# Performance work log

Measured on AMD Instinct MI355X. Metric: run time of the kernel, lower is better.

The kernel has to match this reference:

```python
import jax, jax.numpy as jnp
import numpy as np

D_MODEL = 512
H = 8
DH = D_MODEL // H
P = H * (H - 1) // 2  # 28 head pairs
THRESH = 0.1
B, N = 2, 2048

# pair indices (i<j) in the same row-major order as the nested torch loop
_I_IDX, _J_IDX = np.triu_indices(H, k=1)
I_IDX = jnp.asarray(_I_IDX)
J_IDX = jnp.asarray(_J_IDX)


def setup_inputs() -> dict:
    key = jax.random.key(0)
    ks = jax.random.split(key, 10)
    s = 1.0 / np.sqrt(D_MODEL)
    return {
        "x": jax.random.normal(ks[0], (B, N, D_MODEL), dtype=jnp.float32),
        "Wq": jax.random.normal(ks[1], (D_MODEL, D_MODEL), dtype=jnp.float32) * s,
        "bq": jnp.zeros((D_MODEL,), dtype=jnp.float32),
        "Wk": jax.random.normal(ks[2], (D_MODEL, D_MODEL), dtype=jnp.float32) * s,
        "bk": jnp.zeros((D_MODEL,), dtype=jnp.float32),
        "Wv": jax.random.normal(ks[3], (D_MODEL, D_MODEL), dtype=jnp.float32) * s,
        "bv": jnp.zeros((D_MODEL,), dtype=jnp.float32),
        "Wo": jax.random.normal(ks[4], (D_MODEL, D_MODEL), dtype=jnp.float32) * s,
        "bo": jnp.zeros((D_MODEL,), dtype=jnp.float32),
        # stacked restriction maps: (P, DH_out, DH_in), Linear(bias=False)
        "Wr": jax.random.normal(ks[5], (P, DH, DH), dtype=jnp.float32) / np.sqrt(DH),
        "agreement_scale": jnp.asarray(1.0, dtype=jnp.float32),
    }


def reference(x, Wq, bq, Wk, bk, Wv, bv, Wo, bo, Wr, agreement_scale):
    b, n, d = x.shape
    # projections (torch Linear: y = x @ W.T + b), split into heads -> (B,H,N,DH)
    q = (x @ Wq.T + bq).reshape(b, n, H, DH).transpose(0, 2, 1, 3)
    k = (x @ Wk.T + bk).reshape(b, n, H, DH).transpose(0, 2, 1, 3)
    v = (x @ Wv.T + bv).reshape(b, n, H, DH).transpose(0, 2, 1, 3)

    scores = jnp.einsum("bhnd,bhmd->bhnm", q, k) / jnp.sqrt(jnp.asarray(DH, x.dtype))
    attn = jax.nn.softmax(scores, axis=-1)
    head_out = jnp.einsum("bhnm,bhmd->bhnd", attn, v)  # (B,H,N,DH)

    # --- pairwise restriction-map agreement, fully batched over the P pairs ---
    hi = head_out[:, I_IDX]  # (B,P,N,DH)
    hj = head_out[:, J_IDX]  # (B,P,N,DH)
    ri = jnp.einsum("bpnd,ped->bpne", hi, Wr)  # per-pair Linear(bias=False)
    diff = jnp.linalg.norm(ri - hj, axis=-1).mean(axis=-1)  # (B,P)
    score = jnp.exp(-diff * agreement_scale / THRESH)  # (B,P)

    agreement = jnp.zeros((b, H, H), dtype=x.dtype)
    agreement = agreement.at[:, I_IDX, J_IDX].set(score)
    agreement = agreement.at[:, J_IDX, I_IDX].set(score)
    diag = jnp.arange(H)
    agreement = agreement.at[:, diag, diag].set(1.0)

    # --- consensus aggregation ---
    offdiag = 1.0 - jnp.eye(H, dtype=x.dtype)
    consensus = (agreement * offdiag).sum(axis=-1) / (H - 1)  # (B,H)
    filtered = consensus * (consensus > THRESH).astype(x.dtype)
    weights = jax.nn.softmax(filtered + 1e-10, axis=-1)  # (B,H)

    agg = (head_out * weights[:, :, None, None]).sum(axis=1)  # (B,N,DH)
    agg = jnp.tile(agg, (1, 1, H))  # torch .repeat(1,1,H) -> (B,N,D)
    return agg @ Wo.T + bo
```

## Files before the change

### kernel.cpp

```cpp
#include <hip/hip_runtime.h>
#include <hip/hip_bf16.h>
#include <stdint.h>

typedef __attribute__((ext_vector_type(8))) short bf16x8;
typedef __attribute__((ext_vector_type(4))) float f32x4;
typedef __attribute__((ext_vector_type(4))) unsigned short u16x4;

#define LDS_SWZ(row, col) (((((col) >> 3) ^ ((row) & 7)) << 4))

__device__ __forceinline__ unsigned short f2bf(float f) {
  union { float f; unsigned u; } v; v.f = f;
  unsigned r = v.u + 0x7FFFu + ((v.u >> 16) & 1u);
  return (unsigned short)(r >> 16);
}
__device__ __forceinline__ float bf2f(unsigned short h) {
  union { unsigned u; float f; } v; v.u = ((unsigned)h) << 16;
  return v.f;
}
__device__ __forceinline__ unsigned pk2bf(float a, float b) {
  __hip_bfloat162 h2 = __float22bfloat162_rn(float2{a, b});
  unsigned u; __builtin_memcpy(&u, &h2, 4); return u;
}
__device__ __forceinline__ void gld_lds16(const void* g, void* l) {
  __builtin_amdgcn_global_load_lds((const __attribute__((address_space(1))) void*)g,
                                   (__attribute__((address_space(3))) void*)l, 16, 0, 0);
}

__global__ void k_prep(const float* __restrict__ x, const float* __restrict__ wq,
                       const float* __restrict__ wk, const float* __restrict__ wv,
                       const float* __restrict__ wr, const float* __restrict__ wo,
                       unsigned short* __restrict__ xb, unsigned short* __restrict__ wb,
                       unsigned short* __restrict__ wrb, unsigned short* __restrict__ wsb) {
  int q = blockIdx.x * blockDim.x + threadIdx.x;
  if (q >= 749568) {
    int t = q - 749568;
    if (t >= 512 * 64) return;
    int e = t >> 6, d = t & 63;
    float s = 0.f;
#pragma unroll
    for (int qq = 0; qq < 8; ++qq) s += wo[e * 512 + qq * 64 + d];
    wsb[t] = f2bf(s);
    return;
  }
  const float* src; unsigned short* dst; int off;
  if (q < 524288)      { src = x;  dst = xb;          off = q; }
  else if (q < 589824) { src = wq; dst = wb;          off = q - 524288; }
  else if (q < 655360) { src = wk; dst = wb + 262144; off = q - 589824; }
  else if (q < 720896) { src = wv; dst = wb + 524288; off = q - 655360; }
  else                 { src = wr; dst = wrb;         off = q - 720896; }
  float4 v = ((const float4*)src)[off];
  u16x4 o; o.x = f2bf(v.x); o.y = f2bf(v.y); o.z = f2bf(v.z); o.w = f2bf(v.w);
  ((u16x4*)dst)[off] = o;
}

__global__ __launch_bounds__(256) void k_qkv(
    const unsigned short* __restrict__ xb, const unsigned short* __restrict__ wb,
    const float* __restrict__ bq, const float* __restrict__ bk, const float* __restrict__ bv,
    unsigned short* __restrict__ qb, unsigned short* __restrict__ kb,
    unsigned short* __restrict__ vtb) {
  __shared__ alignas(16) unsigned char As[2][128 * 128];
  __shared__ alignas(16) unsigned char Bs[2][64 * 128];
  const int tid = threadIdx.x;
  const int wave = tid >> 6, lane = tid & 63;
  const int rowbase = blockIdx.x * 128;
  const int colbase = blockIdx.y * 64;
  const int z = blockIdx.z;
  const unsigned short* W = wb + z * 512 * 512;
  const float* bias = (z == 0) ? bq : ((z == 1) ? bk : bv);
  f32x4 acc[2][4] = {};

#define QKV_STAGE(buf, kt_)                                                            \
  do {                                                                                 \
    _Pragma("unroll") for (int i_ = 0; i_ < 4; ++i_) {                                 \
      const int L_ = i_ * 256 + tid;                                                   \
      const int row_ = L_ >> 3, pos_ = L_ & 7;                                         \
      gld_lds16(xb + (rowbase + row_) * 512 + (kt_) * 64 + ((pos_ ^ (row_ & 7)) << 3), \
                As[buf] + (i_ * 256 + wave * 64) * 16);                                \
    }                                                                                  \
    _Pragma("unroll") for (int i_ = 0; i_ < 2; ++i_) {                                 \
      const int L_ = i_ * 256 + tid;                                                   \
      const int row_ = L_ >> 3, pos_ = L_ & 7;                                         \
      gld_lds16(W + (colbase + row_) * 512 + (kt_) * 64 + ((pos_ ^ (row_ & 7)) << 3),  \
                Bs[buf] + (i_ * 256 + wave * 64) * 16);                                \
    }                                                                                  \
  } while (0)

  QKV_STAGE(0, 0);
  __syncthreads();
  for (int kt = 0; kt < 8; ++kt) {
    const int cur = kt & 1;
    if (kt < 7) QKV_STAGE(cur ^ 1, kt + 1);
#pragma unroll
    for (int kc = 0; kc < 2; ++kc) {
      bf16x8 af[2], bfr[4];
#pragma unroll
      for (int mq = 0; mq < 2; ++mq) {
        const int row = wave * 32 + mq * 16 + (lane & 15);
        const int col = kc * 32 + ((lane >> 4) << 3);
        af[mq] = *(const bf16x8*)(As[cur] + row * 128 + LDS_SWZ(row, col));
      }
#pragma unroll
      for (int nq = 0; nq < 4; ++nq) {
        const int row = nq * 16 + (lane & 15);
        const int col = kc * 32 + ((lane >> 4) << 3);
        bfr[nq] = *(const bf16x8*)(Bs[cur] + row * 128 + LDS_SWZ(row, col));
      }
#pragma unroll
      for (int mq = 0; mq < 2; ++mq)
#pragma unroll
        for (int nq = 0; nq < 4; ++nq)
          acc[mq][nq] = __builtin_amdgcn_mfma_f32_16x16x32_bf16(af[mq], bfr[nq], acc[mq][nq], 0, 0, 0);
    }
    __syncthreads();
  }
  const float qs = 0.18033688011112043f;
#pragma unroll
  for (int mq = 0; mq < 2; ++mq)
#pragma unroll
    for (int nq = 0; nq < 4; ++nq)
#pragma unroll
      for (int r = 0; r < 4; ++r) {
        const int grow = rowbase + wave * 32 + mq * 16 + ((lane >> 4) << 2) + r;
        const int col = colbase + nq * 16 + (lane & 15);
        float v = acc[mq][nq][r] + bias[col];
        const int b = grow >> 11, n = grow & 2047;
        const int h = col >> 6, dh = col & 63;
        if (z == 0)      qb[(((b << 3) + h) * 2048 + n) * 64 + dh] = f2bf(v * qs);
        else if (z == 1) kb[(((b << 3) + h) * 2048 + n) * 64 + dh] = f2bf(v);
        else             vtb[((((b << 3) + h) << 6) + dh) * 2048 + n] = f2bf(v);
      }
}

__global__ __launch_bounds__(512, 4) void k_attn(
    const unsigned short* __restrict__ qb, const unsigned short* __restrict__ kb,
    const unsigned short* __restrict__ vtb, unsigned short* __restrict__ hob) {
  __shared__ alignas(16) unsigned char smem[81920];
  const int tid = threadIdx.x, wave = tid >> 6, lane = tid & 63;
  const int team = wave >> 2, w4 = wave & 3;
  const int ttid = tid & 255;
  const int bh = blockIdx.x >> 5;
  const int qt = blockIdx.x & 31;
  const int n0 = qt * 64 + w4 * 16;
  const int lq = lane & 15, lg = lane >> 4;
  unsigned char* Kt = smem + team * 32768;
  unsigned char* Vt = Kt + 16384;
  unsigned char* pw = smem + 65536 + wave * 2048;
  const unsigned short* kbase = kb + bh * 2048 * 64;
  const unsigned short* vbase = vtb + bh * 64 * 2048;
  bf16x8 qf[2];
#pragma unroll
  for (int kc = 0; kc < 2; ++kc)
    qf[kc] = *(const bf16x8*)(qb + (bh * 2048 + n0 + lq) * 64 + kc * 32 + (lg << 3));
  f32x4 oacc[4] = {};
  float mrun = -1e30f, lpart = 0.f;

#define ATTN_STAGE(buf, T_)                                                        \
  do {                                                                             \
    _Pragma("unroll") for (int i_ = 0; i_ < 2; ++i_) {                             \
      const int L_ = i_ * 256 + ttid;                                              \
      const int row_ = L_ >> 3, pos_ = L_ & 7;                                     \
      gld_lds16(kbase + ((T_) * 64 + row_) * 64 + ((pos_ ^ (row_ & 7)) << 3),      \
                Kt + (buf) * 8192 + (i_ * 256 + w4 * 64) * 16);                    \
      gld_lds16(vbase + row_ * 2048 + (T_) * 64 + ((pos_ ^ (row_ & 7)) << 3),      \
                Vt + (buf) * 8192 + (i_ * 256 + w4 * 64) * 16);                    \
    }                                                                              \
  } while (0)

  ATTN_STAGE(0, team * 16);
  __syncthreads();
  for (int t = 0; t < 16; ++t) {
    const int cur = t & 1;
    if (t < 15) ATTN_STAGE(cur ^ 1, team * 16 + t + 1);
    f32x4 s[4];
#pragma unroll
    for (int mc = 0; mc < 4; ++mc) {
      f32x4 zz = {};
#pragma unroll
      for (int kc = 0; kc < 2; ++kc) {
        const int row = mc * 16 + lq;
        const int col = kc * 32 + (lg << 3);
        bf16x8 kf = *(const bf16x8*)(Kt + cur * 8192 + row * 128 + LDS_SWZ(row, col));
        zz = __builtin_amdgcn_mfma_f32_16x16x32_bf16(kf, qf[kc], zz, 0, 0, 0);
      }
      s[mc] = zz;
    }
    float lm = s[0][0];
#pragma unroll
    for (int mc = 0; mc < 4; ++mc)
#pragma unroll
      for (int r = 0; r < 4; ++r) lm = fmaxf(lm, s[mc][r]);
    if (__any(lm > mrun + 8.f)) {
      float v = fmaxf(lm, __shfl_xor(lm, 16));
      v = fmaxf(v, __shfl_xor(v, 32));
      float mnew = fmaxf(mrun, v);
      float sc = exp2f(mrun - mnew);
      mrun = mnew; lpart *= sc;
      float sco[4];
#pragma unroll
      for (int r = 0; r < 4; ++r) sco[r] = __shfl(sc, (lane & 48) | ((lg << 2) + r));
#pragma unroll
      for (int c2 = 0; c2 < 4; ++c2) {
        f32x4 o = oacc[c2];
#pragma unroll
        for (int r = 0; r < 4; ++r) o[r] *= sco[r];
        oacc[c2] = o;
      }
    }
    float pl[4][4];
#pragma unroll
    for (int mc = 0; mc < 4; ++mc) {
      float ps = 0.f;
#pragma unroll
      for (int r = 0; r < 4; ++r) { float p = exp2f(s[mc][r] - mrun); pl[mc][r] = p; ps += p; }
      lpart += ps;
      const int kk = mc * 16 + (lg << 2);
      uint2 pkd = { pk2bf(pl[mc][0], pl[mc][1]), pk2bf(pl[mc][2], pl[mc][3]) };
      *(uint2*)(pw + lq * 128 + LDS_SWZ(lq, kk) + ((kk & 7) << 1)) = pkd;
    }
    bf16x8 pa[2];
#pragma unroll
    for (int kc = 0; kc < 2; ++kc)
      pa[kc] = *(const bf16x8*)(pw + lq * 128 + LDS_SWZ(lq, kc * 32 + (lg << 3)));
#pragma unroll
    for (int c2 = 0; c2 < 4; ++c2) {
      f32x4 o = oacc[c2];
#pragma unroll
      for (int kc = 0; kc < 2; ++kc) {
        const int row = c2 * 16 + lq;
        const int col = kc * 32 + (lg << 3);
        bf16x8 vf = *(const bf16x8*)(Vt + cur * 8192 + row * 128 + LDS_SWZ(row, col));
        o = __builtin_amdgcn_mfma_f32_16x16x32_bf16(pa[kc], vf, o, 0, 0, 0);
      }
      oacc[c2] = o;
    }
    __syncthreads();
  }
  float ltot = lpart + __shfl_xor(lpart, 16);
  ltot += __shfl_xor(ltot, 32);
  float m_o[4], l_o[4];
#pragma unroll
  for (int r = 0; r < 4; ++r) {
    const int src = (lane & 48) | ((lg << 2) + r);
    m_o[r] = __shfl(mrun, src);
    l_o[r] = __shfl(ltot, src);
  }
  float* ex = (float*)smem;
  float* px = ex + (w4 * 64 + lane) * 25;
  if (team == 1) {
#pragma unroll
    for (int c2 = 0; c2 < 4; ++c2)
#pragma unroll
      for (int r = 0; r < 4; ++r) px[c2 * 4 + r] = oacc[c2][r];
#pragma unroll
    for (int r = 0; r < 4; ++r) { px[16 + r] = m_o[r]; px[20 + r] = l_o[r]; }
  }
  __syncthreads();
  if (team == 0) {
    float w0[4], w1[4];
#pragma unroll
    for (int r = 0; r < 4; ++r) {
      float m1 = px[16 + r], l1 = px[20 + r];
      float ms = fmaxf(m_o[r], m1);
      float a = exp2f(m_o[r] - ms), b = exp2f(m1 - ms);
      float li = 1.f / (a * l_o[r] + b * l1);
      w0[r] = a * li; w1[r] = b * li;
    }
#pragma unroll
    for (int c2 = 0; c2 < 4; ++c2)
#pragma unroll
      for (int r = 0; r < 4; ++r) {
        const int n = n0 + (lg << 2) + r;
        const int dh = c2 * 16 + lq;
        float o1 = px[c2 * 4 + r];
        hob[(bh * 2048 + n) * 64 + dh] = f2bf(w0[r] * oacc[c2][r] + w1[r] * o1);
      }
  }
}

__global__ __launch_bounds__(256) void k_pair(const unsigned short* __restrict__ hob,
                                              const unsigned short* __restrict__ wrb,
                                              float* __restrict__ dpart) {
  __shared__ alignas(16) unsigned char Ws[64 * 128];
  __shared__ alignas(16) unsigned char Hj[2][64 * 128];
  __shared__ float red[4];
  const int tid = threadIdx.x, wave = tid >> 6, lane = tid & 63;
  const int chunk = blockIdx.x & 7, bp = blockIdx.x >> 3;
  const int b = bp / 28, p = bp % 28;
  int pp = p, ii = 0;
  while (pp >= 7 - ii) { pp -= 7 - ii; ii++; }
  const int i = ii, j = ii + 1 + pp;
  const unsigned short* hib = hob + ((b * 8 + i) * 2048) * 64;
  const unsigned short* hjb = hob + ((b * 8 + j) * 2048) * 64;

#define PAIR_STAGE(buf, t_)                                                      \
  do {                                                                           \
    _Pragma("unroll") for (int is_ = 0; is_ < 2; ++is_) {                        \
      const int L_ = is_ * 256 + tid;                                            \
      const int row_ = L_ >> 3, pos_ = L_ & 7;                                   \
      gld_lds16(hjb + ((t_) * 64 + row_) * 64 + ((pos_ ^ (row_ & 7)) << 3),      \
                Hj[buf] + (is_ * 256 + wave * 64) * 16);                         \
    }                                                                            \
  } while (0)

#pragma unroll
  for (int is = 0; is < 2; ++is) {
    const int L = is * 256 + tid;
    const int row = L >> 3, pos = L & 7;
    gld_lds16(wrb + (p * 64 + row) * 64 + ((pos ^ (row & 7)) << 3), Ws + (is * 256 + wave * 64) * 16);
  }
  PAIR_STAGE(0, chunk * 4);
  __syncthreads();
  bf16x8 wf[4][2];
#pragma unroll
  for (int c = 0; c < 4; ++c)
#pragma unroll
    for (int kc = 0; kc < 2; ++kc) {
      const int row = c * 16 + (lane & 15);
      const int col = kc * 32 + ((lane >> 4) << 3);
      wf[c][kc] = *(const bf16x8*)(Ws + row * 128 + LDS_SWZ(row, col));
    }
  float wacc = 0.f;
  for (int t = 0; t < 4; ++t) {
    const int tt = chunk * 4 + t;
    const int cur = t & 1;
    if (t < 3) PAIR_STAGE(cur ^ 1, tt + 1);
    const int rbase = tt * 64 + wave * 16;
    f32x4 ri[4] = {};
#pragma unroll
    for (int kc = 0; kc < 2; ++kc) {
      bf16x8 hf = *(const bf16x8*)(hib + (rbase + (lane & 15)) * 64 + kc * 32 + ((lane >> 4) << 3));
#pragma unroll
      for (int c = 0; c < 4; ++c)
        ri[c] = __builtin_amdgcn_mfma_f32_16x16x32_bf16(hf, wf[c][kc], ri[c], 0, 0, 0);
    }
#pragma unroll
    for (int r = 0; r < 4; ++r) {
      const int row = wave * 16 + ((lane >> 4) << 2) + r;
      float ss = 0.f;
#pragma unroll
      for (int c = 0; c < 4; ++c) {
        const int col = c * 16 + (lane & 15);
        float hv = bf2f(*(const unsigned short*)(Hj[cur] + (row & 63) * 128 + LDS_SWZ(row & 63, col) + ((col & 7) << 1)));
        float d = ri[c][r] - hv;
        ss += d * d;
      }
#pragma unroll
      for (int off = 1; off < 16; off <<= 1) ss += __shfl_xor(ss, off);
      if ((lane & 15) == 0) wacc += sqrtf(ss);
    }
    __syncthreads();
  }
  float tot = __shfl(wacc, 0) + __shfl(wacc, 16) + __shfl(wacc, 32) + __shfl(wacc, 48);
  if (lane == 0) red[wave] = tot;
  __syncthreads();
  if (tid == 0) dpart[blockIdx.x] = red[0] + red[1] + red[2] + red[3];
}

__global__ __launch_bounds__(256) void k_agg(const unsigned short* __restrict__ hob,
                                             const float* __restrict__ dpart,
                                             const float* __restrict__ scal,
                                             unsigned short* __restrict__ aggb) {
  __shared__ float sc_s[2][28];
  __shared__ float filt[2][8];
  __shared__ float wts_s[16];
  const int tid = threadIdx.x;
  if (tid < 56) {
    int bb = tid / 28, pp = tid % 28;
    int base = (bb * 28 + pp) * 8;
    float diff = 0.f;
#pragma unroll
    for (int c = 0; c < 8; ++c) diff += dpart[base + c];
    diff /= 2048.f;
    sc_s[bb][pp] = expf(-diff * scal[0] / 0.1f);
  }
  __syncthreads();
  if (tid < 16) {
    int bb = tid / 8, h = tid % 8;
    float cons = 0.f;
    for (int h2 = 0; h2 < 8; ++h2)
      if (h2 != h) {
        int i_ = h < h2 ? h : h2, j_ = h < h2 ? h2 : h;
        int pp = i_ * (15 - i_) / 2 + (j_ - i_ - 1);
        cons += sc_s[bb][pp];
      }
    cons /= 7.f;
    filt[bb][h] = (cons > 0.1f) ? cons : 0.f;
  }
  __syncthreads();
  if (tid < 16) {
    int bb = tid / 8, h = tid % 8;
    float m = -1e30f;
    for (int h2 = 0; h2 < 8; ++h2) m = fmaxf(m, filt[bb][h2] + 1e-10f);
    float s = 0.f;
    for (int h2 = 0; h2 < 8; ++h2) s += expf(filt[bb][h2] + 1e-10f - m);
    wts_s[tid] = expf(filt[bb][h] + 1e-10f - m) / s;
  }
  __syncthreads();
  int t = blockIdx.x * blockDim.x + tid;
  if (t >= 4096 * 8) return;
  int r = t >> 3, dblk = t & 7;
  int b = r >> 11, n = r & 2047;
  float acc[8] = {};
#pragma unroll
  for (int h = 0; h < 8; ++h) {
    float w = wts_s[b * 8 + h];
    bf16x8 v = *(const bf16x8*)(hob + (((b * 8 + h) << 11) + n) * 64 + dblk * 8);
#pragma unroll
    for (int e = 0; e < 8; ++e) acc[e] += w * bf2f((unsigned short)v[e]);
  }
  bf16x8 o;
#pragma unroll
  for (int e = 0; e < 8; ++e) o[e] = (short)f2bf(acc[e]);
  *(bf16x8*)(aggb + r * 64 + dblk * 8) = o;
}

__global__ __launch_bounds__(256) void k_out(const unsigned short* __restrict__ aggb,
                                             const unsigned short* __restrict__ wsb,
                                             const float* __restrict__ bo,
                                             float* __restrict__ out) {
  __shared__ alignas(16) unsigned char Ws[64 * 128];
  const int tid = threadIdx.x, wave = tid >> 6, lane = tid & 63;
  const int rowb = blockIdx.x * 64, colb = blockIdx.y * 64;
#pragma unroll
  for (int is = 0; is < 2; ++is) {
    const int L = is * 256 + tid;
    const int row = L >> 3, pos = L & 7;
    gld_lds16(wsb + (colb + row) * 64 + ((pos ^ (row & 7)) << 3), Ws + (is * 256 + wave * 64) * 16);
  }
  __syncthreads();
  bf16x8 af[2];
#pragma unroll
  for (int kc = 0; kc < 2; ++kc)
    af[kc] = *(const bf16x8*)(aggb + (rowb + wave * 16 + (lane & 15)) * 64 + kc * 32 + ((lane >> 4) << 3));
  f32x4 acc[4] = {};
#pragma unroll
  for (int c = 0; c < 4; ++c)
#pragma unroll
    for (int kc = 0; kc < 2; ++kc) {
      const int row = c * 16 + (lane & 15);
      const int col = kc * 32 + ((lane >> 4) << 3);
      bf16x8 wfr = *(const bf16x8*)(Ws + row * 128 + LDS_SWZ(row, col));
      acc[c] = __builtin_amdgcn_mfma_f32_16x16x32_bf16(af[kc], wfr, acc[c], 0, 0, 0);
    }
#pragma unroll
  for (int c = 0; c < 4; ++c)
#pragma unroll
    for (int r = 0; r < 4; ++r) {
      const int grow = rowb + wave * 16 + ((lane >> 4) << 2) + r;
      const int col = colb + c * 16 + (lane & 15);
      out[grow * 512 + col] = acc[c][r] + bo[col];
    }
}

extern "C" void kernel_launch(void* const* d_in, const int* in_sizes, int n_in,
                              void* d_out, int out_size, void* d_ws, size_t ws_size,
                              hipStream_t stream) {
  const float* x  = (const float*)d_in[0];
  const float* Wq = (const float*)d_in[1];
  const float* bq = (const float*)d_in[2];
  const float* Wk = (const float*)d_in[3];
  const float* bk = (const float*)d_in[4];
  const float* Wv = (const float*)d_in[5];
  const float* bv = (const float*)d_in[6];
  const float* Wo = (const float*)d_in[7];
  const float* bo = (const float*)d_in[8];
  const float* Wr = (const float*)d_in[9];
  const float* ascale = (const float*)d_in[10];
  float* out = (float*)d_out;

  char* ws = (char*)d_ws;
  unsigned short* xb   = (unsigned short*)(ws);
  unsigned short* qb   = (unsigned short*)(ws + (4u << 20));
  unsigned short* kb   = (unsigned short*)(ws + (8u << 20));
  unsigned short* vtb  = (unsigned short*)(ws + (12u << 20));
  unsigned short* hob  = (unsigned short*)(ws + (16u << 20));
  unsigned short* wb   = (unsigned short*)(ws + (20u << 20));
  unsigned short* wrb  = (unsigned short*)(ws + (20u << 20) + 3u * 512 * 512 * 2);
  unsigned short* wsb  = (unsigned short*)(ws + (20u << 20) + 3u * 512 * 512 * 2 + 28u * 64 * 64 * 2);
  unsigned short* aggb = (unsigned short*)(ws + (22u << 20));
  float* dpart = (float*)(ws + (23u << 20));

  k_prep<<<3056, 256, 0, stream>>>(x, Wq, Wk, Wv, Wr, Wo, xb, wb, wrb, wsb);
  k_qkv<<<dim3(32, 8, 3), 256, 0, stream>>>(xb, wb, bq, bk, bv, qb, kb, vtb);
  k_attn<<<512, 512, 0, stream>>>(qb, kb, vtb, hob);
  k_pair<<<448, 256, 0, stream>>>(hob, wrb, dpart);
  k_agg<<<128, 256, 0, stream>>>(hob, dpart, ascale, aggb);
  k_out<<<dim3(64, 8), 256, 0, stream>>>(aggb, wsb, bo, out);
}
```

Measured before the change: 78.78 us.

## Process two query fragments per wave in attention to reuse K/V tiles

Each attention wave now handles 32 query rows (two 16-row fragments) instead of 16. Every K and V fragment read from LDS feeds two MFMAs, which halves the number of blocks and the K/V staging traffic per query. The change also adds s_setprio around the MFMA sections, uses a simpler unswizzled P layout in LDS, and interleaves blocks across heads. In exchange it needs more registers and 96KB of LDS per block, which lowers occupancy.

```diff
diff --git a/kernel.cpp b/kernel.cpp
--- a/kernel.cpp
+++ b/kernel.cpp
@@ -131,28 +131,30 @@
       }
 }
 
-__global__ __launch_bounds__(512, 4) void k_attn(
+__global__ __launch_bounds__(512, 2) void k_attn(
     const unsigned short* __restrict__ qb, const unsigned short* __restrict__ kb,
     const unsigned short* __restrict__ vtb, unsigned short* __restrict__ hob) {
-  __shared__ alignas(16) unsigned char smem[81920];
+  __shared__ alignas(16) unsigned char smem[98304];
   const int tid = threadIdx.x, wave = tid >> 6, lane = tid & 63;
-  const int team = wave >> 2, w4 = wave & 3;
+  const int team = wave >> 2, qsub = wave & 3;
   const int ttid = tid & 255;
-  const int bh = blockIdx.x >> 5;
-  const int qt = blockIdx.x & 31;
-  const int n0 = qt * 64 + w4 * 16;
+  const int bh = blockIdx.x & 15;
+  const int qt = blockIdx.x >> 4;
+  const int n0 = qt * 128 + qsub * 32;
   const int lq = lane & 15, lg = lane >> 4;
   unsigned char* Kt = smem + team * 32768;
   unsigned char* Vt = Kt + 16384;
-  unsigned char* pw = smem + 65536 + wave * 2048;
+  unsigned char* Ps = smem + 65536 + wave * 4096;
   const unsigned short* kbase = kb + bh * 2048 * 64;
   const unsigned short* vbase = vtb + bh * 64 * 2048;
-  bf16x8 qf[2];
-#pragma unroll
-  for (int kc = 0; kc < 2; ++kc)
-    qf[kc] = *(const bf16x8*)(qb + (bh * 2048 + n0 + lq) * 64 + kc * 32 + (lg << 3));
-  f32x4 oacc[4] = {};
-  float mrun = -1e30f, lpart = 0.f;
+  bf16x8 qf[2][2];
+#pragma unroll
+  for (int f = 0; f < 2; ++f)
+#pragma unroll
+    for (int kc = 0; kc < 2; ++kc)
+      qf[f][kc] = *(const bf16x8*)(qb + (bh * 2048 + n0 + f * 16 + lq) * 64 + kc * 32 + (lg << 3));
+  f32x4 oacc[2][4] = {};
+  float mrun[2] = {-1e30f, -1e30f}, lpart[2] = {0.f, 0.f};
 
 #define ATTN_STAGE(buf, T_)                                                        \
   do {                                                                             \
@@ -160,9 +162,9 @@
       const int L_ = i_ * 256 + ttid;                                              \
       const int row_ = L_ >> 3, pos_ = L_ & 7;                                     \
       gld_lds16(kbase + ((T_) * 64 + row_) * 64 + ((pos_ ^ (row_ & 7)) << 3),      \
-                Kt + (buf) * 8192 + (i_ * 256 + w4 * 64) * 16);                    \
+                Kt + (buf) * 8192 + (i_ * 256 + qsub * 64) * 16);                  \
       gld_lds16(vbase + row_ * 2048 + (T_) * 64 + ((pos_ ^ (row_ & 7)) << 3),      \
-                Vt + (buf) * 8192 + (i_ * 256 + w4 * 64) * 16);                    \
+                Vt + (buf) * 8192 + (i_ * 256 + qsub * 64) * 16);                  \
     }                                                                              \
   } while (0)
 
@@ -171,109 +173,135 @@
   for (int t = 0; t < 16; ++t) {
     const int cur = t & 1;
     if (t < 15) ATTN_STAGE(cur ^ 1, team * 16 + t + 1);
-    f32x4 s[4];
-#pragma unroll
-    for (int mc = 0; mc < 4; ++mc) {
-      f32x4 zz = {};
+    f32x4 s[2][4] = {};
+    __builtin_amdgcn_s_setprio(1);
+#pragma unroll
+    for (int mc = 0; mc < 4; ++mc)
 #pragma unroll
       for (int kc = 0; kc < 2; ++kc) {
         const int row = mc * 16 + lq;
         const int col = kc * 32 + (lg << 3);
         bf16x8 kf = *(const bf16x8*)(Kt + cur * 8192 + row * 128 + LDS_SWZ(row, col));
-        zz = __builtin_amdgcn_mfma_f32_16x16x32_bf16(kf, qf[kc], zz, 0, 0, 0);
-      }
-      s[mc] = zz;
-    }
-    float lm = s[0][0];
-#pragma unroll
-    for (int mc = 0; mc < 4; ++mc)
-#pragma unroll
-      for (int r = 0; r < 4; ++r) lm = fmaxf(lm, s[mc][r]);
-    if (__any(lm > mrun + 8.f)) {
-      float v = fmaxf(lm, __shfl_xor(lm, 16));
-      v = fmaxf(v, __shfl_xor(v, 32));
-      float mnew = fmaxf(mrun, v);
-      float sc = exp2f(mrun - mnew);
-      mrun = mnew; lpart *= sc;
-      float sco[4];
-#pragma unroll
-      for (int r = 0; r < 4; ++r) sco[r] = __shfl(sc, (lane & 48) | ((lg << 2) + r));
-#pragma unroll
-      for (int c2 = 0; c2 < 4; ++c2) {
-        f32x4 o = oacc[c2];
-#pragma unroll
-        for (int r = 0; r < 4; ++r) o[r] *= sco[r];
-        oacc[c2] = o;
-      }
-    }
-    float pl[4][4];
-#pragma unroll
-    for (int mc = 0; mc < 4; ++mc) {
-      float ps = 0.f;
-#pragma unroll
-      for (int r = 0; r < 4; ++r) { float p = exp2f(s[mc][r] - mrun); pl[mc][r] = p; ps += p; }
-      lpart += ps;
-      const int kk = mc * 16 + (lg << 2);
-      uint2 pkd = { pk2bf(pl[mc][0], pl[mc][1]), pk2bf(pl[mc][2], pl[mc][3]) };
-      *(uint2*)(pw + lq * 128 + LDS_SWZ(lq, kk) + ((kk & 7) << 1)) = pkd;
-    }
-    bf16x8 pa[2];
-#pragma unroll
-    for (int kc = 0; kc < 2; ++kc)
-      pa[kc] = *(const bf16x8*)(pw + lq * 128 + LDS_SWZ(lq, kc * 32 + (lg << 3)));
-#pragma unroll
-    for (int c2 = 0; c2 < 4; ++c2) {
-      f32x4 o = oacc[c2];
+        s[0][mc] = __builtin_amdgcn_mfma_f32_16x16x32_bf16(kf, qf[0][kc], s[0][mc], 0, 0, 0);
+        s[1][mc] = __builtin_amdgcn_mfma_f32_16x16x32_bf16(kf, qf[1][kc], s[1][mc], 0, 0, 0);
+      }
+    __builtin_amdgcn_s_setprio(0);
+    float lm[2];
+#pragma unroll
+    for (int f = 0; f < 2; ++f) {
+      float a = fmaxf(fmaxf(s[f][0][0], s[f][0][1]), fmaxf(s[f][0][2], s[f][0][3]));
+      float b = fmaxf(fmaxf(s[f][1][0], s[f][1][1]), fmaxf(s[f][1][2], s[f][1][3]));
+      float c = fmaxf(fmaxf(s[f][2][0], s[f][2][1]), fmaxf(s[f][2][2], s[f][2][3]));
+      float d = fmaxf(fmaxf(s[f][3][0], s[f][3][1]), fmaxf(s[f][3][2], s[f][3][3]));
+      lm[f] = fmaxf(fmaxf(a, b), fmaxf(c, d));
+    }
+    if (__any((lm[0] > mrun[0] + 8.f) | (lm[1] > mrun[1] + 8.f))) {
+#pragma unroll
+      for (int f = 0; f < 2; ++f) {
+        float v = fmaxf(lm[f], __shfl_xor(lm[f], 16));
+        v = fmaxf(v, __shfl_xor(v, 32));
+        float mnew = fmaxf(mrun[f], v);
+        float sc = exp2f(mrun[f] - mnew);
+        mrun[f] = mnew; lpart[f] *= sc;
+        float sco[4];
+#pragma unroll
+        for (int r = 0; r < 4; ++r) sco[r] = __shfl(sc, (lane & 48) | ((lg << 2) + r));
+#pragma unroll
+        for (int c2 = 0; c2 < 4; ++c2) {
+          f32x4 o = oacc[f][c2];
+#pragma unroll
+          for (int r = 0; r < 4; ++r) o[r] *= sco[r];
+          oacc[f][c2] = o;
+        }
+      }
+    }
+#pragma unroll
+    for (int f = 0; f < 2; ++f) {
+      unsigned char* pf = Ps + f * 2048;
+#pragma unroll
+      for (int mc = 0; mc < 4; ++mc) {
+        float p0 = exp2f(s[f][mc][0] - mrun[f]);
+        float p1 = exp2f(s[f][mc][1] - mrun[f]);
+        float p2 = exp2f(s[f][mc][2] - mrun[f]);
+        float p3 = exp2f(s[f][mc][3] - mrun[f]);
+        lpart[f] += (p0 + p1) + (p2 + p3);
+        *(uint2*)(pf + (mc * 4 + lg) * 128 + lq * 8) = uint2{pk2bf(p0, p1), pk2bf(p2, p3)};
+      }
+    }
+    bf16x8 pa[2][2];
+#pragma unroll
+    for (int f = 0; f < 2; ++f) {
+      unsigned char* pf = Ps + f * 2048;
+#pragma unroll
+      for (int kc = 0; kc < 2; ++kc) {
+        uint2 a = *(const uint2*)(pf + (kc * 8 + lg * 2) * 128 + lq * 8);
+        uint2 b = *(const uint2*)(pf + (kc * 8 + lg * 2 + 1) * 128 + lq * 8);
+        union { uint4 u; bf16x8 v; } cv; cv.u = uint4{a.x, a.y, b.x, b.y};
+        pa[f][kc] = cv.v;
+      }
+    }
+    __builtin_amdgcn_s_setprio(1);
+#pragma unroll
+    for (int c2 = 0; c2 < 4; ++c2)
 #pragma unroll
       for (int kc = 0; kc < 2; ++kc) {
         const int row = c2 * 16 + lq;
         const int col = kc * 32 + (lg << 3);
         bf16x8 vf = *(const bf16x8*)(Vt + cur * 8192 + row * 128 + LDS_SWZ(row, col));
-        o = __builtin_amdgcn_mfma_f32_16x16x32_bf16(pa[kc], vf, o, 0, 0, 0);
-      }
-      oacc[c2] = o;
-    }
+        oacc[0][c2] = __builtin_amdgcn_mfma_f32_16x16x32_bf16(pa[0][kc], vf, oacc[0][c2], 0, 0, 0);
+        oacc[1][c2] = __builtin_amdgcn_mfma_f32_16x16x32_bf16(pa[1][kc], vf, oacc[1][c2], 0, 0, 0);
+      }
+    __builtin_amdgcn_s_setprio(0);
     __syncthreads();
   }
-  float ltot = lpart + __shfl_xor(lpart, 16);
-  ltot += __shfl_xor(ltot, 32);
-  float m_o[4], l_o[4];
-#pragma unroll
-  for (int r = 0; r < 4; ++r) {
-    const int src = (lane & 48) | ((lg << 2) + r);
-    m_o[r] = __shfl(mrun, src);
-    l_o[r] = __shfl(ltot, src);
-  }
-  float* ex = (float*)smem;
-  float* px = ex + (w4 * 64 + lane) * 25;
+  float m_o[2][4], l_o[2][4];
+#pragma unroll
+  for (int f = 0; f < 2; ++f) {
+    float v = lpart[f] + __shfl_xor(lpart[f], 16);
+    v += __shfl_xor(v, 32);
+#pragma unroll
+    for (int r = 0; r < 4; ++r) {
+      const int src = (lane & 48) | ((lg << 2) + r);
+      m_o[f][r] = __shfl(mrun[f], src);
+      l_o[f][r] = __shfl(v, src);
+    }
+  }
+  __syncthreads();
+  float* px = (float*)smem + (qsub * 64 + lane) * 49;
   if (team == 1) {
 #pragma unroll
-    for (int c2 = 0; c2 < 4; ++c2)
-#pragma unroll
-      for (int r = 0; r < 4; ++r) px[c2 * 4 + r] = oacc[c2][r];
-#pragma unroll
-    for (int r = 0; r < 4; ++r) { px[16 + r] = m_o[r]; px[20 + r] = l_o[r]; }
+    for (int f = 0; f < 2; ++f) {
+#pragma unroll
+      for (int c2 = 0; c2 < 4; ++c2)
+#pragma unroll
+        for (int r = 0; r < 4; ++r) px[f * 16 + c2 * 4 + r] = oacc[f][c2][r];
+#pragma unroll
+      for (int r = 0; r < 4; ++r) { px[32 + f * 8 + r] = m_o[f][r]; px[36 + f * 8 + r] = l_o[f][r]; }
+    }
   }
   __syncthreads();
   if (team == 0) {
-    float w0[4], w1[4];
-#pragma unroll
-    for (int r = 0; r < 4; ++r) {
-      float m1 = px[16 + r], l1 = px[20 + r];
-      float ms = fmaxf(m_o[r], m1);
-      float a = exp2f(m_o[r] - ms), b = exp2f(m1 - ms);
-      float li = 1.f / (a * l_o[r] + b * l1);
-      w0[r] = a * li; w1[r] = b * li;
-    }
-#pragma unroll
-    for (int c2 = 0; c2 < 4; ++c2)
+#pragma unroll
+    for (int f = 0; f < 2; ++f) {
+      float w0[4], w1[4];
 #pragma unroll
       for (int r = 0; r < 4; ++r) {
-        const int n = n0 + (lg << 2) + r;
-        const int dh = c2 * 16 + lq;
-        float o1 = px[c2 * 4 + r];
-        hob[(bh * 2048 + n) * 64 + dh] = f2bf(w0[r] * oacc[c2][r] + w1[r] * o1);
-      }
+        float m1 = px[32 + f * 8 + r], l1 = px[36 + f * 8 + r];
+        float ms = fmaxf(m_o[f][r], m1);
+        float a = exp2f(m_o[f][r] - ms), b = exp2f(m1 - ms);
+        float li = 1.f / (a * l_o[f][r] + b * l1);
+        w0[r] = a * li; w1[r] = b * li;
+      }
+#pragma unroll
+      for (int c2 = 0; c2 < 4; ++c2)
+#pragma unroll
+        for (int r = 0; r < 4; ++r) {
+          const int n = n0 + f * 16 + (lg << 2) + r;
+          const int dh = c2 * 16 + lq;
+          float o1 = px[f * 16 + c2 * 4 + r];
+          hob[(bh * 2048 + n) * 64 + dh] = f2bf(w0[r] * oacc[f][c2][r] + w1[r] * o1);
+        }
+    }
   }
 }
 
@@ -482,7 +510,7 @@
 
   k_prep<<<3056, 256, 0, stream>>>(x, Wq, Wk, Wv, Wr, Wo, xb, wb, wrb, wsb);
   k_qkv<<<dim3(32, 8, 3), 256, 0, stream>>>(xb, wb, bq, bk, bv, qb, kb, vtb);
-  k_attn<<<512, 512, 0, stream>>>(qb, kb, vtb, hob);
+  k_attn<<<256, 512, 0, stream>>>(qb, kb, vtb, hob);
   k_pair<<<448, 256, 0, stream>>>(hob, wrb, dpart);
   k_agg<<<128, 256, 0, stream>>>(hob, dpart, ascale, aggb);
   k_out<<<dim3(64, 8), 256, 0, stream>>>(aggb, wsb, bo, out);
```

After: 79.58 us. No clear change (+1.0%).
